# Performance work log

Hardware: AMD Instinct MI355X
Metric: run time of the kernel (lower is better)

The kernel has to match this reference:

```python
import jax, jax.numpy as jnp
import numpy as np

N_NODES = 100_000
N_HYPEREDGES = 200_000
NNZ = 2_000_000
D = 64
H = 32
KEEP_RATIO = 0.5


def setup_inputs() -> dict:
    key = jax.random.key(0)
    ks = jax.random.split(key, 5)
    x = jax.random.normal(ks[0], (N_NODES, D), jnp.float32)
    V_idx = jax.random.randint(ks[1], (NNZ,), 0, N_NODES)
    E_idx = jax.random.randint(ks[2], (NNZ,), 0, N_HYPEREDGES)
    W1 = jax.random.normal(ks[3], (2 * D, H), jnp.float32) * (1.0 / np.sqrt(2 * D))
    b1 = jnp.zeros((H,), jnp.float32)
    W2 = jax.random.normal(ks[4], (H, 1), jnp.float32) * (1.0 / np.sqrt(H))
    b2 = jnp.zeros((1,), jnp.float32)
    return dict(x=x, V_idx=V_idx, E_idx=E_idx, W1=W1, b1=b1, W2=W2, b2=b2)


def _segment_mean(vals, idx, num_segments):
    # index_add sum / clamped count, matching reduce_incidence_to_edge / index_mean
    s = jax.ops.segment_sum(vals, idx, num_segments=num_segments)
    c = jax.ops.segment_sum(jnp.ones((vals.shape[0],), vals.dtype), idx,
                            num_segments=num_segments)
    c = jnp.clip(c, 1.0, None)
    if vals.ndim == 2:
        c = c[:, None]
    return s / c


def reference(x, V_idx, E_idx, W1, b1, W2, b2):
    xv = x[V_idx]                                   # [nnz, D] gather
    edge_feats = _segment_mean(xv, E_idx, N_HYPEREDGES)  # [E, D]
    pair = jnp.concatenate([xv, edge_feats[E_idx]], axis=-1)  # [nnz, 2D]
    h = jax.nn.relu(pair @ W1 + b1)                 # [nnz, H]
    probs = jax.nn.sigmoid((h @ W2 + b2)[:, 0])     # [nnz]

    k = max(1, int(KEEP_RATIO * NNZ))
    keep_ids = jax.lax.top_k(probs, k)[1]           # is_test=True path (deterministic)
    hard = jnp.zeros_like(probs).at[keep_ids].set(1.0)
    soft = jax.lax.stop_gradient(hard - probs) + probs  # straight-through

    edge_probs = _segment_mean(jax.lax.stop_gradient(probs), E_idx, N_HYPEREDGES)
    edge_soft = _segment_mean(soft, E_idx, N_HYPEREDGES)
    edge_hard = (_segment_mean(hard, E_idx, N_HYPEREDGES) > 0).astype(jnp.float32)
    return (probs, soft, hard, edge_probs, edge_soft, edge_hard)
```

## Files before the change

kernel.cpp:

```cpp
#include <hip/hip_runtime.h>
#include <math.h>

#define N_NODES   100000
#define N_EDGES   200000
#define NNZ       2000000
#define K_KEEP    1000000
#define BANDCAP   131072
#define TIECAP    4096
#define DELTA     1.0e-3f
#define SCAN_BLOCKS 196
#define USCALE (4294967296.0 / 4.0e-3)

#define SC_PASSES 8
#define SC_EPP    (N_EDGES / SC_PASSES)
#define SC_BLOCKS 2048

#define OFF_PAB   ((size_t)0)
#define OFF_PB32  ((size_t)25600000)
#define OFF_VJ    ((size_t)33600000)
#define OFF_RANK  ((size_t)49600000)
#define OFF_EOFF  ((size_t)57600000)
#define OFF_CUR   ((size_t)58400000)
#define OFF_BS    ((size_t)59200000)
#define OFF_BANDP ((size_t)59201024)
#define OFF_BANDJ ((size_t)59725312)
#define OFF_BANDE ((size_t)60249600)
#define OFF_BANDV ((size_t)60773888)
#define OFF_BANDK ((size_t)61298176)
#define OFF_TIEK  ((size_t)62346752)
#define OFF_TIEJ  ((size_t)62379520)
#define OFF_TIEP  ((size_t)62395904)
#define OFF_FLAG  ((size_t)62412288)
#define OFF_ECNT  ((size_t)64412288)
#define OFF_HIST  ((size_t)65212288)
#define OFF_ST    ((size_t)65245056)
#define ZERO_OFF  OFF_FLAG
#define ZERO_LEN  ((size_t)(65245312 - 62412288))

struct SelState {
    unsigned int B1;
    unsigned int rem1;
    float lo_edge, hi_edge;
    unsigned int bB1;
    unsigned int brem1;
    unsigned int bU0;
    unsigned int brem2;
    unsigned int _pad0[8];
    unsigned int n_hi;      unsigned int _pad1[15];
    unsigned int band_n;    unsigned int _pad2[15];
    unsigned int tie_n;     unsigned int _pad3[15];
};

__device__ __forceinline__ unsigned int band_u32(double key, float lo) {
    double t = (key - (double)lo) * USCALE;
    t = t < 0.0 ? 0.0 : (t > 4294967295.0 ? 4294967295.0 : t);
    return (unsigned int)t;
}

__global__ void proj_kernel(const float* __restrict__ x, const float* __restrict__ W1,
                            float2* __restrict__ p_ab2) {
    __shared__ float sW[128 * 32];
    __shared__ float sx[8][64];
    for (int t = threadIdx.x; t < 128 * 32; t += 256) sW[t] = W1[t];
    int base = blockIdx.x * 8;
    for (int t = threadIdx.x; t < 512; t += 256) {
        int n = t >> 6, d = t & 63;
        int g = base + n;
        sx[n][d] = (g < N_NODES) ? x[(size_t)g * 64 + d] : 0.f;
    }
    __syncthreads();
    int ln = threadIdx.x >> 5;
    int k  = threadIdx.x & 31;
    int node = base + ln;
    if (node >= N_NODES) return;
    float sa = 0.f, sb = 0.f;
    for (int d = 0; d < 64; ++d) {
        float xv = sx[ln][d];
        sa += xv * sW[d * 32 + k];
        sb += xv * sW[(64 + d) * 32 + k];
    }
    p_ab2[(size_t)node * 32 + k] = make_float2(sa, sb);
}

__global__ void count_rank_kernel(const int* __restrict__ E, unsigned int* __restrict__ edge_cnt,
                                  unsigned int* __restrict__ rank) {
    unsigned int base = blockIdx.x * 2048 + threadIdx.x;
    int ev[8];
    unsigned int rr[8];
    #pragma unroll
    for (int c = 0; c < 8; ++c) {
        unsigned int j = base + 256u * c;
        if (j < NNZ) ev[c] = E[j];
    }
    #pragma unroll
    for (int c = 0; c < 8; ++c) {
        unsigned int j = base + 256u * c;
        if (j < NNZ) rr[c] = atomicAdd(&edge_cnt[ev[c]], 1u);
    }
    #pragma unroll
    for (int c = 0; c < 8; ++c) {
        unsigned int j = base + 256u * c;
        if (j < NNZ) rank[j] = rr[c];
    }
}

__global__ void scanA_kernel(const unsigned int* __restrict__ edge_cnt,
                             unsigned int* __restrict__ edge_off, unsigned int* __restrict__ bsums) {
    __shared__ unsigned int s[256];
    int tid = threadIdx.x;
    int base = blockIdx.x * 1024 + tid * 4;
    unsigned int v0 = (base + 0 < N_EDGES) ? edge_cnt[base + 0] : 0u;
    unsigned int v1 = (base + 1 < N_EDGES) ? edge_cnt[base + 1] : 0u;
    unsigned int v2 = (base + 2 < N_EDGES) ? edge_cnt[base + 2] : 0u;
    unsigned int v3 = (base + 3 < N_EDGES) ? edge_cnt[base + 3] : 0u;
    unsigned int tsum = v0 + v1 + v2 + v3;
    s[tid] = tsum;
    __syncthreads();
    for (int off = 1; off < 256; off <<= 1) {
        unsigned int t = (tid >= off) ? s[tid - off] : 0u;
        __syncthreads();
        s[tid] += t;
        __syncthreads();
    }
    unsigned int excl = s[tid] - tsum;
    if (base + 0 < N_EDGES) edge_off[base + 0] = excl;
    if (base + 1 < N_EDGES) edge_off[base + 1] = excl + v0;
    if (base + 2 < N_EDGES) edge_off[base + 2] = excl + v0 + v1;
    if (base + 3 < N_EDGES) edge_off[base + 3] = excl + v0 + v1 + v2;
    if (tid == 255) bsums[blockIdx.x] = s[255];
}

__global__ void scanB_kernel(unsigned int* __restrict__ bsums) {
    __shared__ unsigned int s[256];
    int tid = threadIdx.x;
    unsigned int v = (tid < SCAN_BLOCKS) ? bsums[tid] : 0u;
    s[tid] = v;
    __syncthreads();
    for (int off = 1; off < 256; off <<= 1) {
        unsigned int t = (tid >= off) ? s[tid - off] : 0u;
        __syncthreads();
        s[tid] += t;
        __syncthreads();
    }
    if (tid < SCAN_BLOCKS) bsums[tid] = s[tid] - v;
}

__global__ void scanC_kernel(unsigned int* __restrict__ edge_off, const unsigned int* __restrict__ bsums) {
    int i = blockIdx.x * 256 + threadIdx.x;
    if (i >= N_EDGES) return;
    edge_off[i] = edge_off[i] + bsums[i >> 10];
}

__global__ void scatter_kernel(const int* __restrict__ V, const int* __restrict__ E,
                               const unsigned int* __restrict__ edge_off,
                               const unsigned int* __restrict__ rank,
                               uint2* __restrict__ vj) {
    unsigned int pass = blockIdx.x & 7u;
    unsigned int q    = blockIdx.x >> 3;
    unsigned int elo  = pass * SC_EPP;
    const unsigned int stride = (SC_BLOCKS / 8) * 256;
    for (unsigned int j = q * 256u + threadIdx.x; j < NNZ; j += stride) {
        unsigned int e = (unsigned int)__builtin_nontemporal_load(E + j);
        if (e - elo < (unsigned int)SC_EPP) {
            unsigned int pp = edge_off[e] + __builtin_nontemporal_load(rank + j);
            unsigned int v  = (unsigned int)__builtin_nontemporal_load(V + j);
            vj[pp] = make_uint2(v, j);
        }
    }
}

__global__ void edge_logit_kernel(const uint2* __restrict__ vj,
                                  const unsigned int* __restrict__ edge_off,
                                  const unsigned int* __restrict__ edge_cnt,
                                  const float2* __restrict__ p_ab2,
                                  const float* __restrict__ b1, const float* __restrict__ W2,
                                  const float* __restrict__ b2,
                                  float* __restrict__ probs_b, float* __restrict__ o_ep) {
    __shared__ float sa[4][32 * 32];
    __shared__ float slog[4][32];
    __shared__ unsigned int sv[4][32];
    int e = blockIdx.x * 4 + (threadIdx.x >> 6);
    if (e >= N_EDGES) return;
    int w    = threadIdx.x >> 6;
    int lane = threadIdx.x & 63;
    int k    = lane & 31;
    unsigned int half = (unsigned int)(lane >> 5);

    unsigned int off = edge_off[e];
    unsigned int deg = edge_cnt[e];
    unsigned int mind = deg < 32u ? deg : 32u;

    if ((unsigned int)lane < mind) sv[w][lane] = vj[off + lane].x;

    float bacc = 0.f;
    unsigned int i = half;
    for (; i + 6u < mind; i += 8u) {
        unsigned int v0 = sv[w][i];
        unsigned int v1 = sv[w][i + 2u];
        unsigned int v2 = sv[w][i + 4u];
        unsigned int v3 = sv[w][i + 6u];
        float2 r0 = p_ab2[(size_t)v0 * 32u + k];
        float2 r1 = p_ab2[(size_t)v1 * 32u + k];
        float2 r2 = p_ab2[(size_t)v2 * 32u + k];
        float2 r3 = p_ab2[(size_t)v3 * 32u + k];
        sa[w][(i)      * 32 + k] = r0.x;
        sa[w][(i + 2u) * 32 + k] = r1.x;
        sa[w][(i + 4u) * 32 + k] = r2.x;
        sa[w][(i + 6u) * 32 + k] = r3.x;
        bacc += (r0.y + r1.y) + (r2.y + r3.y);
    }
    for (; i + 2u < mind; i += 4u) {
        unsigned int v0 = sv[w][i];
        unsigned int v1 = sv[w][i + 2u];
        float2 r0 = p_ab2[(size_t)v0 * 32u + k];
        float2 r1 = p_ab2[(size_t)v1 * 32u + k];
        sa[w][(i)      * 32 + k] = r0.x;
        sa[w][(i + 2u) * 32 + k] = r1.x;
        bacc += r0.y + r1.y;
    }
    for (; i < mind; i += 2u) {
        unsigned int v = sv[w][i];
        float2 r = p_ab2[(size_t)v * 32u + k];
        sa[w][i * 32 + k] = r.x;
        bacc += r.y;
    }
    for (i = 32u + half; i < deg; i += 2u) {
        unsigned int v = vj[off + i].x;
        bacc += p_ab2[(size_t)v * 32u + k].y;
    }

    float cc  = (float)(deg > 1u ? deg : 1u);
    float emk = (bacc + __shfl_xor(bacc, 32)) / cc + b1[k];
    float w2k = W2[k];
    float b2v = b2[0];
    float prsum = 0.f;

    i = half;
    for (; i + 2u < mind; i += 4u) {
        float h0 = sa[w][(i)      * 32 + k] + emk;
        float h1 = sa[w][(i + 2u) * 32 + k] + emk;
        h0 = h0 > 0.f ? h0 : 0.f;
        h1 = h1 > 0.f ? h1 : 0.f;
        float t0 = h0 * w2k;
        float t1 = h1 * w2k;
        #pragma unroll
        for (int o = 16; o > 0; o >>= 1) {
            t0 += __shfl_down(t0, o, 32);
            t1 += __shfl_down(t1, o, 32);
        }
        if (k == 0) { slog[w][i] = t0; slog[w][i + 2u] = t1; }
    }
    for (; i < mind; i += 2u) {
        float hk = sa[w][i * 32 + k] + emk;
        hk = hk > 0.f ? hk : 0.f;
        float t = hk * w2k;
        #pragma unroll
        for (int o = 16; o > 0; o >>= 1) t += __shfl_down(t, o, 32);
        if (k == 0) slog[w][i] = t;
    }
    if ((unsigned int)lane < mind) {
        float pr = 1.f / (1.f + __expf(-(slog[w][lane] + b2v)));
        probs_b[off + lane] = pr;
        prsum = pr;
    }
    for (i = 32u + half; i < deg; i += 2u) {
        unsigned int v = vj[off + i].x;
        float hk = p_ab2[(size_t)v * 32u + k].x + emk;
        hk = hk > 0.f ? hk : 0.f;
        float t = hk * w2k;
        #pragma unroll
        for (int o = 16; o > 0; o >>= 1) t += __shfl_down(t, o, 32);
        if (k == 0) {
            float pr = 1.f / (1.f + __expf(-(t + b2v)));
            probs_b[off + i] = pr;
            prsum += pr;
        }
    }
    #pragma unroll
    for (int o = 32; o > 0; o >>= 1) prsum += __shfl_down(prsum, o, 64);
    if (lane == 0) o_ep[e] = prsum / cc;
}

__global__ void hist1_kernel(const float* __restrict__ probs_b, unsigned int* __restrict__ hist) {
    __shared__ unsigned int lh[2048];
    for (int t = threadIdx.x; t < 2048; t += 256) lh[t] = 0;
    __syncthreads();
    for (unsigned int i = blockIdx.x * 256 + threadIdx.x; i < NNZ; i += gridDim.x * 256) {
        unsigned int key = __float_as_uint(probs_b[i]);
        atomicAdd(&lh[key >> 21], 1u);
    }
    __syncthreads();
    for (int t = threadIdx.x; t < 2048; t += 256)
        if (lh[t]) atomicAdd(&hist[t], lh[t]);
}

__global__ void hist2_kernel(const float* __restrict__ probs_b, const SelState* __restrict__ st,
                             unsigned int* __restrict__ hist) {
    __shared__ unsigned int lh[2048];
    for (int t = threadIdx.x; t < 2048; t += 256) lh[t] = 0;
    __syncthreads();
    unsigned int B1 = st->B1;
    for (unsigned int i = blockIdx.x * 256 + threadIdx.x; i < NNZ; i += gridDim.x * 256) {
        unsigned int key = __float_as_uint(probs_b[i]);
        if ((key >> 21) == B1) atomicAdd(&lh[(key >> 10) & 2047u], 1u);
    }
    __syncthreads();
    for (int t = threadIdx.x; t < 2048; t += 256)
        if (lh[t]) atomicAdd(&hist[2048 + t], lh[t]);
}

__global__ void scan_sel_kernel(const unsigned int* __restrict__ hist, SelState* __restrict__ st, int which) {
    __shared__ unsigned int csum[256];
    int t = threadIdx.x;
    unsigned int target = (which == 0) ? (unsigned int)K_KEEP : st->rem1;
    const unsigned int* h = hist + (which ? 2048 : 0);
    unsigned int b[8];
    unsigned int s = 0;
    #pragma unroll
    for (int i = 0; i < 8; ++i) { b[i] = h[t * 8 + i]; s += b[i]; }
    csum[t] = s;
    __syncthreads();
    for (int off = 1; off < 256; off <<= 1) {
        unsigned int v = (t + off < 256) ? csum[t + off] : 0u;
        __syncthreads();
        csum[t] += v;
        __syncthreads();
    }
    unsigned int above = csum[t] - s;
    if (above < target && target <= above + s) {
        unsigned int rem = target - above;
        unsigned int cum = 0;
        #pragma unroll
        for (int i = 7; i >= 0; --i) {
            if (rem <= cum + b[i]) {
                unsigned int bin = (unsigned int)(t * 8 + i);
                if (which == 0) { st->B1 = bin; st->rem1 = rem - cum; }
                else {
                    unsigned int P = (st->B1 << 21) | (bin << 10);
                    st->lo_edge = __uint_as_float(P) - DELTA;
                    st->hi_edge = __uint_as_float(P + 1024u) + DELTA;
                }
                break;
            }
            cum += b[i];
        }
    }
}

__global__ void bandsel_kernel(const float* __restrict__ probs_b, const int* __restrict__ E,
                               const uint2* __restrict__ vj,
                               SelState* __restrict__ st,
                               unsigned int* __restrict__ band_p, unsigned int* __restrict__ band_j,
                               unsigned int* __restrict__ band_e, unsigned int* __restrict__ band_v) {
    __shared__ unsigned int whi[4], wband[4];
    __shared__ unsigned int sbase, scur;
    float hi = st->hi_edge, lo = st->lo_edge;
    unsigned int nhi = 0, nband = 0;
    for (unsigned int p = blockIdx.x * 256 + threadIdx.x; p < NNZ; p += gridDim.x * 256) {
        float pk = probs_b[p];
        if (pk > hi) nhi++;
        else if (pk >= lo) nband++;
    }
    #pragma unroll
    for (int o = 32; o > 0; o >>= 1) {
        nhi   += __shfl_down(nhi, o);
        nband += __shfl_down(nband, o);
    }
    if ((threadIdx.x & 63) == 0) { whi[threadIdx.x >> 6] = nhi; wband[threadIdx.x >> 6] = nband; }
    __syncthreads();
    if (threadIdx.x == 0) {
        unsigned int th = whi[0] + whi[1] + whi[2] + whi[3];
        unsigned int tb = wband[0] + wband[1] + wband[2] + wband[3];
        if (th) atomicAdd(&st->n_hi, th);
        sbase = tb ? atomicAdd(&st->band_n, tb) : 0u;
        scur = 0;
    }
    __syncthreads();
    for (unsigned int p = blockIdx.x * 256 + threadIdx.x; p < NNZ; p += gridDim.x * 256) {
        float pk = probs_b[p];
        if (pk <= hi && pk >= lo) {
            unsigned int s = sbase + atomicAdd(&scur, 1u);
            if (s < BANDCAP) {
                uint2 t = vj[p];
                band_p[s] = p;
                band_j[s] = t.y;
                band_e[s] = (unsigned int)E[t.y];
                band_v[s] = t.x;
            }
        }
    }
}

__global__ void rescue_kernel(const uint2* __restrict__ vj,
                              const unsigned int* __restrict__ edge_off,
                              const unsigned int* __restrict__ edge_cnt,
                              const float* __restrict__ x, const float* __restrict__ W1,
                              const float* __restrict__ b1, const float* __restrict__ W2,
                              const float* __restrict__ b2,
                              const unsigned int* __restrict__ band_e,
                              const unsigned int* __restrict__ band_v,
                              const SelState* __restrict__ st,
                              unsigned long long* __restrict__ band_key) {
    unsigned int n = st->band_n; if (n > BANDCAP) n = BANDCAP;
    if (blockIdx.x * 8 >= n) return;
    __shared__ float sW[128 * 32];
    for (int t = threadIdx.x; t < 128 * 32; t += 256) sW[t] = W1[t];
    __syncthreads();
    unsigned int g = blockIdx.x * 8 + (threadIdx.x >> 5);
    if (g >= n) return;
    int k = threadIdx.x & 31;
    unsigned int v = band_v[g];
    unsigned int e = band_e[g];
    unsigned int off = edge_off[e];
    unsigned int deg = edge_cnt[e];

    const float* xv = x + (size_t)v * 64u;
    double a = 0.0;
    #pragma unroll 8
    for (int d = 0; d < 64; ++d) a += (double)xv[d] * (double)sW[d * 32 + k];
    double bsum = 0.0;
    for (unsigned int m = off; m < off + deg; ++m) {
        const float* xm = x + (size_t)vj[m].x * 64u;
        double acc = 0.0;
        #pragma unroll 8
        for (int d = 0; d < 64; ++d) acc += (double)xm[d] * (double)sW[(64 + d) * 32 + k];
        bsum += acc;
    }
    double cc = (double)(deg > 1u ? deg : 1u);
    double h = a + bsum / cc + (double)b1[k];
    h = h > 0.0 ? h : 0.0;
    double t = h * (double)W2[k];
    #pragma unroll
    for (int o = 16; o > 0; o >>= 1) t += __shfl_down(t, o, 32);
    if (k == 0) {
        double pr = 1.0 / (1.0 + exp(-(t + (double)b2[0])));
        band_key[g] = (unsigned long long)__double_as_longlong(pr);
    }
}

__global__ void bhist1_kernel(const unsigned long long* __restrict__ band_key,
                              const SelState* __restrict__ st, unsigned int* __restrict__ hist) {
    __shared__ unsigned int lh[2048];
    for (int t = threadIdx.x; t < 2048; t += 256) lh[t] = 0;
    __syncthreads();
    unsigned int n = st->band_n; if (n > BANDCAP) n = BANDCAP;
    float lo = st->lo_edge;
    for (unsigned int i = blockIdx.x * 256 + threadIdx.x; i < n; i += gridDim.x * 256) {
        unsigned int u = band_u32(__longlong_as_double((long long)band_key[i]), lo);
        atomicAdd(&lh[u >> 21], 1u);
    }
    __syncthreads();
    for (int t = threadIdx.x; t < 2048; t += 256)
        if (lh[t]) atomicAdd(&hist[4096 + t], lh[t]);
}

__global__ void bhist2_kernel(const unsigned long long* __restrict__ band_key,
                              const SelState* __restrict__ st, unsigned int* __restrict__ hist) {
    __shared__ unsigned int lh[2048];
    for (int t = threadIdx.x; t < 2048; t += 256) lh[t] = 0;
    __syncthreads();
    unsigned int n = st->band_n; if (n > BANDCAP) n = BANDCAP;
    float lo = st->lo_edge;
    unsigned int bB1 = st->bB1;
    for (unsigned int i = blockIdx.x * 256 + threadIdx.x; i < n; i += gridDim.x * 256) {
        unsigned int u = band_u32(__longlong_as_double((long long)band_key[i]), lo);
        if ((u >> 21) == bB1) atomicAdd(&lh[(u >> 10) & 2047u], 1u);
    }
    __syncthreads();
    for (int t = threadIdx.x; t < 2048; t += 256)
        if (lh[t]) atomicAdd(&hist[6144 + t], lh[t]);
}

__global__ void bscan_kernel(const unsigned int* __restrict__ hist, SelState* __restrict__ st, int which) {
    __shared__ unsigned int csum[256];
    int t = threadIdx.x;
    unsigned int target = (which == 0) ? ((unsigned int)K_KEEP - st->n_hi) : st->brem1;
    const unsigned int* h = hist + (which ? 6144 : 4096);
    unsigned int b[8];
    unsigned int s = 0;
    #pragma unroll
    for (int i = 0; i < 8; ++i) { b[i] = h[t * 8 + i]; s += b[i]; }
    csum[t] = s;
    __syncthreads();
    for (int off = 1; off < 256; off <<= 1) {
        unsigned int v = (t + off < 256) ? csum[t + off] : 0u;
        __syncthreads();
        csum[t] += v;
        __syncthreads();
    }
    unsigned int above = csum[t] - s;
    if (above < target && target <= above + s) {
        unsigned int rem = target - above;
        unsigned int cum = 0;
        #pragma unroll
        for (int i = 7; i >= 0; --i) {
            if (rem <= cum + b[i]) {
                unsigned int bin = (unsigned int)(t * 8 + i);
                if (which == 0) { st->bB1 = bin; st->brem1 = rem - cum; }
                else            { st->bU0 = (st->bB1 << 21) | (bin << 10); st->brem2 = rem - cum; }
                break;
            }
            cum += b[i];
        }
    }
}

__global__ void btie_kernel(const unsigned long long* __restrict__ band_key,
                            const unsigned int* __restrict__ band_j,
                            const unsigned int* __restrict__ band_p,
                            SelState* __restrict__ st, unsigned char* __restrict__ flag,
                            unsigned long long* __restrict__ tie_k,
                            unsigned int* __restrict__ tie_j, unsigned int* __restrict__ tie_p) {
    unsigned int n = st->band_n; if (n > BANDCAP) n = BANDCAP;
    unsigned int i = blockIdx.x * 256 + threadIdx.x;
    if (i >= n) return;
    float lo = st->lo_edge;
    unsigned int U0 = st->bU0;
    unsigned long long key = band_key[i];
    unsigned int u = band_u32(__longlong_as_double((long long)key), lo);
    if (u >= U0 + 1024u) {
        flag[band_p[i]] = 2u;
    } else if (u >= U0) {
        unsigned int s = atomicAdd(&st->tie_n, 1u);
        if (s < TIECAP) { tie_k[s] = key; tie_j[s] = band_j[i]; tie_p[s] = band_p[i]; }
    }
}

__global__ void btierank_kernel(const unsigned long long* __restrict__ tie_k,
                                const unsigned int* __restrict__ tie_j,
                                const unsigned int* __restrict__ tie_p,
                                const SelState* __restrict__ st, unsigned char* __restrict__ flag) {
    unsigned int n = st->tie_n; if (n > TIECAP) n = TIECAP;
    unsigned int need = st->brem2;
    for (unsigned int i = threadIdx.x; i < n; i += 256) {
        unsigned long long ki = tie_k[i];
        unsigned int ji = tie_j[i];
        unsigned int r = 0;
        for (unsigned int q = 0; q < n; ++q) {
            unsigned long long kq = tie_k[q];
            if (kq > ki || (kq == ki && tie_j[q] < ji)) r++;
        }
        if (r < need) flag[tie_p[i]] = 2u;
    }
}

__global__ void out_kernel(const float* __restrict__ probs_b, const unsigned char* __restrict__ flag,
                           const int* __restrict__ E, const unsigned int* __restrict__ rank,
                           const unsigned int* __restrict__ edge_off, const SelState* __restrict__ st,
                           float* __restrict__ o_probs, float* __restrict__ o_soft, float* __restrict__ o_hard) {
    unsigned int j = blockIdx.x * 256 + threadIdx.x;
    if (j >= NNZ) return;
    float hi = st->hi_edge;
    unsigned int p = edge_off[E[j]] + rank[j];
    float pk = probs_b[p];
    float hb = (pk > hi || flag[p] == 2u) ? 1.f : 0.f;
    o_probs[j] = pk;
    o_soft[j]  = hb;
    o_hard[j]  = hb;
}

__global__ void edge_out_kernel(const float* __restrict__ probs_b, const unsigned char* __restrict__ flag,
                                const unsigned int* __restrict__ edge_off,
                                const unsigned int* __restrict__ edge_cnt,
                                const SelState* __restrict__ st,
                                float* __restrict__ o_es, float* __restrict__ o_eh) {
    unsigned int e = blockIdx.x * 256 + threadIdx.x;
    if (e >= N_EDGES) return;
    float hi = st->hi_edge;
    unsigned int off = edge_off[e], deg = edge_cnt[e];
    unsigned int cnt = 0;
    for (unsigned int i = 0; i < deg; ++i)
        cnt += (probs_b[off + i] > hi || flag[off + i] == 2u) ? 1u : 0u;
    float cc = (float)(deg > 1u ? deg : 1u);
    o_es[e] = (float)cnt / cc;
    o_eh[e] = cnt ? 1.f : 0.f;
}

extern "C" void kernel_launch(void* const* d_in, const int* in_sizes, int n_in,
                              void* d_out, int out_size, void* d_ws, size_t ws_size,
                              hipStream_t stream) {
    const float* x  = (const float*)d_in[0];
    const int*   V  = (const int*)d_in[1];
    const int*   E  = (const int*)d_in[2];
    const float* W1 = (const float*)d_in[3];
    const float* b1 = (const float*)d_in[4];
    const float* W2 = (const float*)d_in[5];
    const float* b2 = (const float*)d_in[6];

    float* out     = (float*)d_out;
    float* o_probs = out;
    float* o_soft  = out + NNZ;
    float* o_hard  = out + 2 * (size_t)NNZ;
    float* o_ep    = out + 3 * (size_t)NNZ;
    float* o_es    = out + 3 * (size_t)NNZ + N_EDGES;
    float* o_eh    = out + 3 * (size_t)NNZ + 2 * (size_t)N_EDGES;

    char* w = (char*)d_ws;
    float2*             p_ab2    = (float2*)(w + OFF_PAB);
    float*              probs_b  = (float*)(w + OFF_PB32);
    uint2*              vj       = (uint2*)(w + OFF_VJ);
    unsigned int*       rank     = (unsigned int*)(w + OFF_RANK);
    unsigned int*       edge_off = (unsigned int*)(w + OFF_EOFF);
    unsigned int*       bsums    = (unsigned int*)(w + OFF_BS);
    unsigned int*       band_p   = (unsigned int*)(w + OFF_BANDP);
    unsigned int*       band_j   = (unsigned int*)(w + OFF_BANDJ);
    unsigned int*       band_e   = (unsigned int*)(w + OFF_BANDE);
    unsigned int*       band_v   = (unsigned int*)(w + OFF_BANDV);
    unsigned long long* band_key = (unsigned long long*)(w + OFF_BANDK);
    unsigned long long* tie_k    = (unsigned long long*)(w + OFF_TIEK);
    unsigned int*       tie_j    = (unsigned int*)(w + OFF_TIEJ);
    unsigned int*       tie_p    = (unsigned int*)(w + OFF_TIEP);
    unsigned char*      flag     = (unsigned char*)(w + OFF_FLAG);
    unsigned int*       edge_cnt = (unsigned int*)(w + OFF_ECNT);
    unsigned int*       hist     = (unsigned int*)(w + OFF_HIST);
    SelState*           st       = (SelState*)(w + OFF_ST);

    hipMemsetAsync(w + ZERO_OFF, 0, ZERO_LEN, stream);

    proj_kernel<<<(N_NODES + 7) / 8, 256, 0, stream>>>(x, W1, p_ab2);

    count_rank_kernel<<<(NNZ + 2047) / 2048, 256, 0, stream>>>(E, edge_cnt, rank);
    scanA_kernel<<<SCAN_BLOCKS, 256, 0, stream>>>(edge_cnt, edge_off, bsums);
    scanB_kernel<<<1, 256, 0, stream>>>(bsums);
    scanC_kernel<<<(N_EDGES + 255) / 256, 256, 0, stream>>>(edge_off, bsums);
    scatter_kernel<<<SC_BLOCKS, 256, 0, stream>>>(V, E, edge_off, rank, vj);

    edge_logit_kernel<<<(N_EDGES + 3) / 4, 256, 0, stream>>>(vj, edge_off, edge_cnt,
                                                             p_ab2, b1, W2, b2, probs_b, o_ep);

    hist1_kernel<<<1024, 256, 0, stream>>>(probs_b, hist);
    scan_sel_kernel<<<1, 256, 0, stream>>>(hist, st, 0);
    hist2_kernel<<<1024, 256, 0, stream>>>(probs_b, st, hist);
    scan_sel_kernel<<<1, 256, 0, stream>>>(hist, st, 1);

    bandsel_kernel<<<1024, 256, 0, stream>>>(probs_b, E, vj, st,
                                             band_p, band_j, band_e, band_v);
    rescue_kernel<<<BANDCAP / 8, 256, 0, stream>>>(vj, edge_off, edge_cnt, x, W1, b1, W2, b2,
                                                   band_e, band_v, st, band_key);

    bhist1_kernel<<<64, 256, 0, stream>>>(band_key, st, hist);
    bscan_kernel<<<1, 256, 0, stream>>>(hist, st, 0);
    bhist2_kernel<<<64, 256, 0, stream>>>(band_key, st, hist);
    bscan_kernel<<<1, 256, 0, stream>>>(hist, st, 1);
    btie_kernel<<<BANDCAP / 256, 256, 0, stream>>>(band_key, band_j, band_p, st, flag,
                                                   tie_k, tie_j, tie_p);
    btierank_kernel<<<1, 256, 0, stream>>>(tie_k, tie_j, tie_p, st, flag);

    out_kernel<<<(NNZ + 255) / 256, 256, 0, stream>>>(probs_b, flag, E, rank, edge_off, st,
                                                      o_probs, o_soft, o_hard);
    edge_out_kernel<<<(N_EDGES + 255) / 256, 256, 0, stream>>>(probs_b, flag, edge_off, edge_cnt, st,
                                                               o_es, o_eh);
}
```

Measured before the change: 632.2 us.

## Rework edge logit kernel to use float4 gathers with register-held per-incidence partials

The edge logit kernel now splits each wavefront into four 16-lane groups. Each group gathers one node's 32 projected (a,b) pairs as float4 loads, so four incidences are fetched per step instead of two. The per-incidence 'a' partials stay in registers (an 8-entry array) instead of the shared sa buffer, which removes a shared-memory round trip. The logit reduction now needs four shuffle steps instead of five. The cost is higher register pressure and more branching around the unrolled per-group loop.

Result: faster. 613.6 us (-2.9%).

```diff
diff --git a/kernel.cpp b/kernel.cpp
--- a/kernel.cpp
+++ b/kernel.cpp
@@ -176,15 +176,14 @@
                                   const float* __restrict__ b1, const float* __restrict__ W2,
                                   const float* __restrict__ b2,
                                   float* __restrict__ probs_b, float* __restrict__ o_ep) {
-    __shared__ float sa[4][32 * 32];
     __shared__ float slog[4][32];
     __shared__ unsigned int sv[4][32];
     int e = blockIdx.x * 4 + (threadIdx.x >> 6);
     if (e >= N_EDGES) return;
     int w    = threadIdx.x >> 6;
     int lane = threadIdx.x & 63;
-    int k    = lane & 31;
-    unsigned int half = (unsigned int)(lane >> 5);
+    int g    = lane >> 4;
+    int l    = lane & 15;
 
     unsigned int off = edge_off[e];
     unsigned int deg = edge_cnt[e];
@@ -192,87 +191,71 @@
 
     if ((unsigned int)lane < mind) sv[w][lane] = vj[off + lane].x;
 
-    float bacc = 0.f;
-    unsigned int i = half;
-    for (; i + 6u < mind; i += 8u) {
-        unsigned int v0 = sv[w][i];
-        unsigned int v1 = sv[w][i + 2u];
-        unsigned int v2 = sv[w][i + 4u];
-        unsigned int v3 = sv[w][i + 6u];
-        float2 r0 = p_ab2[(size_t)v0 * 32u + k];
-        float2 r1 = p_ab2[(size_t)v1 * 32u + k];
-        float2 r2 = p_ab2[(size_t)v2 * 32u + k];
-        float2 r3 = p_ab2[(size_t)v3 * 32u + k];
-        sa[w][(i)      * 32 + k] = r0.x;
-        sa[w][(i + 2u) * 32 + k] = r1.x;
-        sa[w][(i + 4u) * 32 + k] = r2.x;
-        sa[w][(i + 6u) * 32 + k] = r3.x;
-        bacc += (r0.y + r1.y) + (r2.y + r3.y);
-    }
-    for (; i + 2u < mind; i += 4u) {
-        unsigned int v0 = sv[w][i];
-        unsigned int v1 = sv[w][i + 2u];
-        float2 r0 = p_ab2[(size_t)v0 * 32u + k];
-        float2 r1 = p_ab2[(size_t)v1 * 32u + k];
-        sa[w][(i)      * 32 + k] = r0.x;
-        sa[w][(i + 2u) * 32 + k] = r1.x;
-        bacc += r0.y + r1.y;
-    }
-    for (; i < mind; i += 2u) {
-        unsigned int v = sv[w][i];
-        float2 r = p_ab2[(size_t)v * 32u + k];
-        sa[w][i * 32 + k] = r.x;
-        bacc += r.y;
-    }
-    for (i = 32u + half; i < deg; i += 2u) {
-        unsigned int v = vj[off + i].x;
-        bacc += p_ab2[(size_t)v * 32u + k].y;
-    }
-
-    float cc  = (float)(deg > 1u ? deg : 1u);
-    float emk = (bacc + __shfl_xor(bacc, 32)) / cc + b1[k];
-    float w2k = W2[k];
-    float b2v = b2[0];
-    float prsum = 0.f;
-
-    i = half;
-    for (; i + 2u < mind; i += 4u) {
-        float h0 = sa[w][(i)      * 32 + k] + emk;
-        float h1 = sa[w][(i + 2u) * 32 + k] + emk;
+    float2 w2  = ((const float2*)W2)[l];
+    float2 bb1 = ((const float2*)b1)[l];
+    float  b2v = b2[0];
+
+    float2 aA[8];
+    float2 bacc = make_float2(0.f, 0.f);
+    #pragma unroll 8
+    for (unsigned int m = 0; m < 8u; ++m) {
+        if (4u * m >= mind) break;
+        unsigned int idx = 4u * m + (unsigned int)g;
+        if (idx < mind) {
+            unsigned int v = sv[w][idx];
+            float4 r = reinterpret_cast<const float4*>(p_ab2 + (size_t)v * 32u)[l];
+            aA[m] = make_float2(r.x, r.z);
+            bacc.x += r.y;
+            bacc.y += r.w;
+        } else {
+            aA[m] = make_float2(0.f, 0.f);
+        }
+    }
+    for (unsigned int ii = 32u + (unsigned int)g; ii < deg; ii += 4u) {
+        unsigned int v = vj[off + ii].x;
+        float4 r = reinterpret_cast<const float4*>(p_ab2 + (size_t)v * 32u)[l];
+        bacc.x += r.y;
+        bacc.y += r.w;
+    }
+    bacc.x += __shfl_xor(bacc.x, 16);
+    bacc.y += __shfl_xor(bacc.y, 16);
+    bacc.x += __shfl_xor(bacc.x, 32);
+    bacc.y += __shfl_xor(bacc.y, 32);
+    float cc = (float)(deg > 1u ? deg : 1u);
+    float2 em2 = make_float2(bacc.x / cc + bb1.x, bacc.y / cc + bb1.y);
+
+    #pragma unroll 8
+    for (unsigned int m = 0; m < 8u; ++m) {
+        if (4u * m >= mind) break;
+        unsigned int idx = 4u * m + (unsigned int)g;
+        float h0 = aA[m].x + em2.x;
+        float h1 = aA[m].y + em2.y;
         h0 = h0 > 0.f ? h0 : 0.f;
         h1 = h1 > 0.f ? h1 : 0.f;
-        float t0 = h0 * w2k;
-        float t1 = h1 * w2k;
+        float t = h0 * w2.x + h1 * w2.y;
         #pragma unroll
-        for (int o = 16; o > 0; o >>= 1) {
-            t0 += __shfl_down(t0, o, 32);
-            t1 += __shfl_down(t1, o, 32);
-        }
-        if (k == 0) { slog[w][i] = t0; slog[w][i + 2u] = t1; }
-    }
-    for (; i < mind; i += 2u) {
-        float hk = sa[w][i * 32 + k] + emk;
-        hk = hk > 0.f ? hk : 0.f;
-        float t = hk * w2k;
-        #pragma unroll
-        for (int o = 16; o > 0; o >>= 1) t += __shfl_down(t, o, 32);
-        if (k == 0) slog[w][i] = t;
-    }
+        for (int o = 8; o > 0; o >>= 1) t += __shfl_down(t, o, 16);
+        if (l == 0 && idx < mind) slog[w][idx] = t;
+    }
+    float prsum = 0.f;
     if ((unsigned int)lane < mind) {
         float pr = 1.f / (1.f + __expf(-(slog[w][lane] + b2v)));
         probs_b[off + lane] = pr;
         prsum = pr;
     }
-    for (i = 32u + half; i < deg; i += 2u) {
-        unsigned int v = vj[off + i].x;
-        float hk = p_ab2[(size_t)v * 32u + k].x + emk;
-        hk = hk > 0.f ? hk : 0.f;
-        float t = hk * w2k;
+    for (unsigned int ii = 32u + (unsigned int)g; ii < deg; ii += 4u) {
+        unsigned int v = vj[off + ii].x;
+        float4 r = reinterpret_cast<const float4*>(p_ab2 + (size_t)v * 32u)[l];
+        float h0 = r.x + em2.x;
+        float h1 = r.z + em2.y;
+        h0 = h0 > 0.f ? h0 : 0.f;
+        h1 = h1 > 0.f ? h1 : 0.f;
+        float t = h0 * w2.x + h1 * w2.y;
         #pragma unroll
-        for (int o = 16; o > 0; o >>= 1) t += __shfl_down(t, o, 32);
-        if (k == 0) {
+        for (int o = 8; o > 0; o >>= 1) t += __shfl_down(t, o, 16);
+        if (l == 0) {
             float pr = 1.f / (1.f + __expf(-(t + b2v)));
-            probs_b[off + i] = pr;
+            probs_b[off + ii] = pr;
             prsum += pr;
         }
     }
```
